# Performance work log

Hardware: AMD Instinct MI355X
Metric: run time of the kernel (lower is better)

## Reference

```python
import jax, jax.numpy as jnp
import numpy as np
import math

H, KV, D, HID, WIN = 8, 4, 256, 2048, 1024  # heads, kv heads, head_dim, hidden, sliding window
B, S = 1, 2048

def _rms(x, scale):
    # Gemma3RMSNorm: hardcoded 1e-6 eps, (1+scale) gain
    var = jnp.mean(jnp.square(x), axis=-1, keepdims=True)
    return x * jax.lax.rsqrt(var + 1e-6) * (1.0 + scale)

def _rot_half(x):
    x1, x2 = jnp.split(x, 2, axis=-1)
    return jnp.concatenate((-x2, x1), axis=-1)

def setup_inputs() -> dict:
    key = jax.random.key(0)
    ks = jax.random.split(key, 8)
    x = jax.random.normal(ks[0], (B, S, HID), jnp.float32)
    attn_mask = jnp.ones((B, S), jnp.bool_)
    segment_pos = jnp.broadcast_to(jnp.arange(S, dtype=jnp.int32)[None], (B, S))
    # true RoPE tables, theta=1e6 (Gemma3 global layers)
    inv_freq = 1.0 / (1e6 ** (np.arange(0, D, 2, dtype=np.float32) / D))
    ang = np.arange(S, dtype=np.float32)[:, None] * inv_freq[None, :]  # [S, D/2]
    emb = np.concatenate([ang, ang], axis=-1)                          # [S, D]
    cos = jnp.asarray(np.cos(emb), jnp.float32)[None]                  # [1, S, D]
    sin = jnp.asarray(np.sin(emb), jnp.float32)[None]
    sd = 1.0 / math.sqrt(HID)
    wq = jax.random.normal(ks[1], (HID, H * D), jnp.float32) * sd
    wk = jax.random.normal(ks[2], (HID, KV * D), jnp.float32) * sd
    wv = jax.random.normal(ks[3], (HID, KV * D), jnp.float32) * sd
    wo = jax.random.normal(ks[4], (H * D, HID), jnp.float32) * (1.0 / math.sqrt(H * D))
    q_scale = jnp.zeros((D,), jnp.float32)  # zeros_init as in module
    k_scale = jnp.zeros((D,), jnp.float32)
    return dict(x=x, attn_mask=attn_mask, segment_pos=segment_pos, cos=cos, sin=sin,
                wq=wq, wk=wk, wv=wv, wo=wo, q_scale=q_scale, k_scale=k_scale)

def reference(x, attn_mask, segment_pos, cos, sin, wq, wk, wv, wo, q_scale, k_scale):
    b, s, _ = x.shape
    # projections -> [b, h, s, d]
    q = (x @ wq).reshape(b, s, H, D).transpose(0, 2, 1, 3)
    k = (x @ wk).reshape(b, s, KV, D).transpose(0, 2, 1, 3)
    v = (x @ wv).reshape(b, s, KV, D).transpose(0, 2, 1, 3)
    # per-head QK RMSNorm
    q = _rms(q, q_scale)
    k = _rms(k, k_scale)
    # RoPE (cos/sin broadcast over head axis, unsqueeze_dim=1)
    c, sn = cos[:, None], sin[:, None]
    q = q * c + _rot_half(q) * sn
    k = k * c + _rot_half(k) * sn
    # GQA: repeat-interleave kv heads
    rep = H // KV
    k = jnp.repeat(k, rep, axis=1)
    v = jnp.repeat(v, rep, axis=1)
    scores = jnp.einsum('bhqd,bhkd->bhqk', q, k) / math.sqrt(D)
    # causal + padding mask (q_len > 1 path, no image bidirectional mask)
    causal = jnp.tril(jnp.ones((s, s), jnp.bool_))
    mask = causal[None] & attn_mask[:, None, :]          # [b, q, kv]
    # sliding window mask (prefill: cache positions = arange)
    kvpos = jnp.arange(s)
    pos = segment_pos[:, :, None]
    sliding = (kvpos[None, None] > pos - WIN) & (kvpos[None, None] < pos + WIN)
    full = mask & sliding
    scores = scores + jnp.where(full[:, None], 0.0, -1e37)
    w = jax.nn.softmax(scores.astype(jnp.float32), axis=-1).astype(scores.dtype)
    out = jnp.einsum('bhqk,bhkd->bhqd', w, v)
    out = out.transpose(0, 2, 1, 3).reshape(b, s, H * D)
    return out @ wo
```

## Files before the change

### kernel.cpp

```cpp
#include <hip/hip_runtime.h>
#include <hip/hip_bf16.h>

#define S_LEN 2048
#define HID 2048
#define NH 8
#define NKV 4
#define HD 256
#define WIN 1024

typedef __hip_bfloat16 bf16;
typedef __attribute__((ext_vector_type(8))) short bf16x8;
typedef __attribute__((ext_vector_type(4))) float f32x4;

__device__ __forceinline__ void gld_lds16(void* lds, const void* g) {
    __builtin_amdgcn_global_load_lds(
        (const __attribute__((address_space(1))) unsigned int*)g,
        (__attribute__((address_space(3))) unsigned int*)lds,
        16, 0, 0);
}


__device__ __forceinline__ void transT_body(const float* __restrict__ src, bf16* __restrict__ dst,
                                            int R, int C, int r0, int c0) {
    __shared__ bf16 Ts[64][72];
    const int tid = threadIdx.x;
    {
        const int r = tid >> 2;
        const int cq = (tid & 3) * 16;
#pragma unroll
        for (int j = 0; j < 16; j += 4) {
            float4 v = *(const float4*)&src[(size_t)(r0 + r) * C + c0 + cq + j];
            Ts[cq + j + 0][r] = __float2bfloat16(v.x);
            Ts[cq + j + 1][r] = __float2bfloat16(v.y);
            Ts[cq + j + 2][r] = __float2bfloat16(v.z);
            Ts[cq + j + 3][r] = __float2bfloat16(v.w);
        }
    }
    __syncthreads();
    {
        const int c = tid >> 2;
        const int rq = (tid & 3) * 16;
#pragma unroll
        for (int j = 0; j < 16; j += 8)
            *(uint4*)&dst[(size_t)(c0 + c) * R + r0 + rq + j] = *(const uint4*)&Ts[c][rq + j];
    }
}

__global__ __launch_bounds__(256)
void prep_all(const float* __restrict__ xf, const float* __restrict__ wqf,
              const float* __restrict__ wkf, const float* __restrict__ wvf,
              const float* __restrict__ wof,
              bf16* __restrict__ xb, bf16* __restrict__ wqkvt, bf16* __restrict__ wot) {
    const int bid = blockIdx.x;
    if (bid < 2048) {
        const int i = bid * 256 + threadIdx.x;
        float4 a = ((const float4*)xf)[i * 2];
        float4 b = ((const float4*)xf)[i * 2 + 1];
        union { uint4 v; bf16 h[8]; } u;
        u.h[0] = __float2bfloat16(a.x); u.h[1] = __float2bfloat16(a.y);
        u.h[2] = __float2bfloat16(a.z); u.h[3] = __float2bfloat16(a.w);
        u.h[4] = __float2bfloat16(b.x); u.h[5] = __float2bfloat16(b.y);
        u.h[6] = __float2bfloat16(b.z); u.h[7] = __float2bfloat16(b.w);
        ((uint4*)xb)[i] = u.v;
    } else if (bid < 4096) {
        const int t = bid - 2048;
        const int bx = t & 63, by = t >> 6;
        const float* src; int C, c0, drow0;
        if (bx < 32)      { src = wqf; C = 2048; c0 = bx * 64;        drow0 = bx * 64; }
        else if (bx < 48) { src = wkf; C = 1024; c0 = (bx - 32) * 64; drow0 = 2048 + (bx - 32) * 64; }
        else              { src = wvf; C = 1024; c0 = (bx - 48) * 64; drow0 = 3072 + (bx - 48) * 64; }
        bf16* dshift = wqkvt + ((size_t)drow0 - c0) * HID;
        transT_body(src, dshift, HID, C, by * 64, c0);
    } else {
        const int t = bid - 4096;
        const int bx = t & 31, by = t >> 5;
        transT_body(wof, wot, NH * HD, HID, by * 64, bx * 64);
    }
}

template<int MODE>
__global__ __launch_bounds__(512, 2)
void gemm8p(const bf16* __restrict__ A, const bf16* __restrict__ Bt,
            bf16* __restrict__ Cb,
            bf16* __restrict__ Qo, bf16* __restrict__ Ko, bf16* __restrict__ Vto) {
    extern __shared__ bf16 smem[];
    bf16* AsP = smem;
    bf16* BsP = smem + 3 * 256 * 64;

    const int tid = threadIdx.x;
    const int w = tid >> 6, lane = tid & 63;
    const int lnm = lane & 15, quad = lane >> 4;
    const int wr = w >> 1, wc = w & 1;
    const int r8 = lane >> 3;
    const int swz = ((lane & 7) ^ r8) * 8;

    const int bid = blockIdx.x;
    const int xcd = bid & 7, idx = bid >> 3;
    int m0, n0, kbeg, nt;
    size_t zoff = 0;
    if constexpr (MODE == 1) {
        const int m_t = (xcd >> 2) * 4 + (idx >> 3);
        const int n_t = (xcd & 3) * 8 + (idx & 7);
        m0 = m_t * 256; n0 = n_t * 128; kbeg = 0; nt = 2048 / 64;
    } else {
        const int z   = xcd >> 2;
        const int n_t = (xcd & 3) * 4 + (idx & 3);
        const int m_t = idx >> 2;
        m0 = m_t * 256; n0 = n_t * 128; kbeg = z * 1024; nt = 1024 / 64;
        zoff = (size_t)z * 2048 * 2048;
    }
    const int K = 2048;

    const bf16* pA[4];
#pragma unroll
    for (int g = 0; g < 4; ++g)
        pA[g] = A + (size_t)(m0 + w * 32 + g * 8 + r8) * K + kbeg + swz;
    const bf16* pB[2];
#pragma unroll
    for (int g = 0; g < 2; ++g)
        pB[g] = Bt + (size_t)(n0 + w * 16 + g * 8 + r8) * K + kbeg + swz;
    const int dA = w * 32 * 64;
    const int dB = w * 16 * 64;

#define STG_A(slot, g, t) gld_lds16(AsP + (slot) * 16384 + dA + (g) * 512, pA[g] + (t) * 64)
#define STG_B(slot, g, t) gld_lds16(BsP + (slot) * 8192  + dB + (g) * 512, pB[g] + (t) * 64)
#define LDFRAG(base, row, kh) \
    (*(const bf16x8*)((base) + (row) * 64 + (((((kh) << 2) | quad) ^ ((row) & 7)) << 3)))

    f32x4 acc[4][4];
#pragma unroll
    for (int i = 0; i < 4; ++i)
#pragma unroll
        for (int j = 0; j < 4; ++j) acc[i][j] = (f32x4){0.f, 0.f, 0.f, 0.f};

    STG_A(0, 0, 0); STG_A(0, 1, 0); STG_A(0, 2, 0); STG_A(0, 3, 0);
    STG_B(0, 0, 0); STG_B(0, 1, 0);
    STG_A(1, 0, 1); STG_A(1, 1, 1); STG_A(1, 2, 1); STG_A(1, 3, 1);
    STG_B(1, 0, 1); STG_B(1, 1, 1);
    asm volatile("s_waitcnt vmcnt(6)" ::: "memory");
    __builtin_amdgcn_sched_barrier(0);
    __builtin_amdgcn_s_barrier();

    int sc = 0;
    for (int t = 0; t < nt; ++t) {
        const int ss = (sc == 0) ? 2 : sc - 1;
        const bf16* As_ = AsP + sc * 16384;
        const bf16* Bs_ = BsP + sc * 8192;
        const bool pf = (t + 2 < nt);

        bf16x8 a0[2][2], b[4][2];
#pragma unroll
        for (int tm = 0; tm < 2; ++tm)
#pragma unroll
            for (int kh = 0; kh < 2; ++kh)
                a0[tm][kh] = LDFRAG(As_, wr * 64 + tm * 16 + lnm, kh);
#pragma unroll
        for (int tn = 0; tn < 4; ++tn)
#pragma unroll
            for (int kh = 0; kh < 2; ++kh)
                b[tn][kh] = LDFRAG(Bs_, wc * 64 + tn * 16 + lnm, kh);
        if (pf) { STG_A(ss, 0, t + 2); STG_A(ss, 1, t + 2); STG_B(ss, 0, t + 2); }
        __builtin_amdgcn_s_barrier();
        asm volatile("s_waitcnt lgkmcnt(0)" ::: "memory");
        __builtin_amdgcn_sched_barrier(0);
        __builtin_amdgcn_s_setprio(1);
#pragma unroll
        for (int kh = 0; kh < 2; ++kh)
#pragma unroll
            for (int tm = 0; tm < 2; ++tm)
#pragma unroll
                for (int tn = 0; tn < 4; ++tn)
                    acc[tm][tn] = __builtin_amdgcn_mfma_f32_16x16x32_bf16(
                        a0[tm][kh], b[tn][kh], acc[tm][tn], 0, 0, 0);
        __builtin_amdgcn_s_setprio(0);
        __builtin_amdgcn_s_barrier();

        bf16x8 a1[2][2];
#pragma unroll
        for (int tm = 0; tm < 2; ++tm)
#pragma unroll
            for (int kh = 0; kh < 2; ++kh)
                a1[tm][kh] = LDFRAG(As_, wr * 64 + (tm + 2) * 16 + lnm, kh);
        if (pf) { STG_A(ss, 2, t + 2); STG_A(ss, 3, t + 2); STG_B(ss, 1, t + 2); }
        if (pf) { asm volatile("s_waitcnt vmcnt(6)" ::: "memory"); }
        else    { asm volatile("s_waitcnt vmcnt(0)" ::: "memory"); }
        __builtin_amdgcn_sched_barrier(0);
        __builtin_amdgcn_s_barrier();
        asm volatile("s_waitcnt lgkmcnt(0)" ::: "memory");
        __builtin_amdgcn_sched_barrier(0);
        __builtin_amdgcn_s_setprio(1);
#pragma unroll
        for (int kh = 0; kh < 2; ++kh)
#pragma unroll
            for (int tm = 0; tm < 2; ++tm)
#pragma unroll
                for (int tn = 0; tn < 4; ++tn)
                    acc[tm + 2][tn] = __builtin_amdgcn_mfma_f32_16x16x32_bf16(
                        a1[tm][kh], b[tn][kh], acc[tm + 2][tn], 0, 0, 0);
        __builtin_amdgcn_s_setprio(0);
        __builtin_amdgcn_s_barrier();

        sc = (sc == 2) ? 0 : sc + 1;
    }
#undef STG_A
#undef STG_B
#undef LDFRAG

#pragma unroll
    for (int tm = 0; tm < 4; ++tm)
#pragma unroll
        for (int tn = 0; tn < 4; ++tn)
#pragma unroll
            for (int r = 0; r < 4; ++r) {
                const int row = m0 + wr * 64 + tm * 16 + quad * 4 + r;
                const int col = n0 + wc * 64 + tn * 16 + lnm;
                const float v = acc[tm][tn][r];
                if constexpr (MODE == 2) {
                    Cb[zoff + (size_t)row * 2048 + col] = __float2bfloat16(v);
                } else {
                    if (col < 2048)
                        Qo[(size_t)row * (NH * HD) + col] = __float2bfloat16(v);
                    else if (col < 3072)
                        Ko[(size_t)row * (NKV * HD) + col - 2048] = __float2bfloat16(v);
                    else
                        Vto[(size_t)(col - 3072) * S_LEN + row] = __float2bfloat16(v);
                }
            }
}

__global__ __launch_bounds__(256)
void splitk_add(const bf16* __restrict__ p, float* __restrict__ out) {
    const int i = blockIdx.x * 256 + threadIdx.x;
    union { uint4 v; bf16 h[8]; } a, b;
    a.v = ((const uint4*)p)[i];
    b.v = ((const uint4*)(p + (size_t)2048 * 2048))[i];
    float4 o0, o1;
    o0.x = (float)a.h[0] + (float)b.h[0]; o0.y = (float)a.h[1] + (float)b.h[1];
    o0.z = (float)a.h[2] + (float)b.h[2]; o0.w = (float)a.h[3] + (float)b.h[3];
    o1.x = (float)a.h[4] + (float)b.h[4]; o1.y = (float)a.h[5] + (float)b.h[5];
    o1.z = (float)a.h[6] + (float)b.h[6]; o1.w = (float)a.h[7] + (float)b.h[7];
    ((float4*)out)[i * 2]     = o0;
    ((float4*)out)[i * 2 + 1] = o1;
}

__global__ __launch_bounds__(64)
void rmsrope_kernel(bf16* __restrict__ Q, bf16* __restrict__ Kb,
                    const float* __restrict__ cosb, const float* __restrict__ sinb,
                    const float* __restrict__ qscale, const float* __restrict__ kscale,
                    float qmul) {
    const int p = blockIdx.x;
    const int hg = blockIdx.y;
    const int lane = threadIdx.x;

    bf16* base;
    const float* scale;
    float mul;
    if (hg < NH) { base = Q + (size_t)p * (NH * HD) + hg * HD; scale = qscale; mul = qmul; }
    else         { base = Kb + (size_t)p * (NKV * HD) + (hg - NH) * HD; scale = kscale; mul = 1.f; }

    const int d0 = lane * 2;
    float x0 = (float)base[d0],       x1 = (float)base[d0 + 1];
    float y0 = (float)base[d0 + 128], y1 = (float)base[d0 + 129];

    float ss = x0 * x0 + x1 * x1 + y0 * y0 + y1 * y1;
#pragma unroll
    for (int off = 32; off > 0; off >>= 1) ss += __shfl_xor(ss, off, 64);
    const float r = rsqrtf(ss * (1.0f / (float)HD) + 1e-6f);

    x0 *= r * (1.f + scale[d0]);
    x1 *= r * (1.f + scale[d0 + 1]);
    y0 *= r * (1.f + scale[d0 + 128]);
    y1 *= r * (1.f + scale[d0 + 129]);

    const size_t cb = (size_t)p * HD;
    const float c0 = cosb[cb + d0],       c1 = cosb[cb + d0 + 1];
    const float cA = cosb[cb + d0 + 128], cB = cosb[cb + d0 + 129];
    const float s0 = sinb[cb + d0],       s1 = sinb[cb + d0 + 1];
    const float sA = sinb[cb + d0 + 128], sB = sinb[cb + d0 + 129];

    base[d0]       = __float2bfloat16((x0 * c0 - y0 * s0) * mul);
    base[d0 + 1]   = __float2bfloat16((x1 * c1 - y1 * s1) * mul);
    base[d0 + 128] = __float2bfloat16((y0 * cA + x0 * sA) * mul);
    base[d0 + 129] = __float2bfloat16((y1 * cB + x1 * sB) * mul);
}

#define NCHUNK 4

__device__ __forceinline__ unsigned pkbf(float a, float b) {
    union { bf16 h; unsigned short u; } ca, cb;
    ca.h = __float2bfloat16(a); cb.h = __float2bfloat16(b);
    return (unsigned)ca.u | ((unsigned)cb.u << 16);
}

__global__ __launch_bounds__(256)
void attn_mfma(const bf16* __restrict__ Q, const bf16* __restrict__ K,
               const bf16* __restrict__ Vt, bf16* __restrict__ Op,
               float2* __restrict__ ml) {
    __shared__ bf16 Ks[2][32][256];
    __shared__ bf16 Vs[256][32];
    const int qt = blockIdx.x, h = blockIdx.y, chunk = blockIdx.z, kvh = h >> 1;
    const int tid = threadIdx.x, w = tid >> 6, lane = tid & 63;
    const int lnm = lane & 15, quad = lane >> 4;

    bf16x8 qf[8];
    const int qrow = qt * 64 + w * 16 + lnm;
#pragma unroll
    for (int s = 0; s < 8; ++s)
        qf[s] = *(const bf16x8*)&Q[(size_t)qrow * HID + h * HD + s * 32 + quad * 8];

    f32x4 o[16];
#pragma unroll
    for (int i = 0; i < 16; ++i) o[i] = (f32x4){0.f, 0.f, 0.f, 0.f};
    float M = -3e38f, L = 0.f;

    const int ktlo = (qt >= 16) ? (2 * qt - 32) : 0;
    const int kthi = 2 * qt + 1;
    const int ntile = kthi - ktlo + 1;
    const int c0 = ktlo + (chunk * ntile) / NCHUNK;
    const int c1 = ktlo + ((chunk + 1) * ntile) / NCHUNK - 1;

    const int srow = w * 8 + (lane >> 5);
    const int sunit = lane & 31;
    const bf16* kg = K + (size_t)kvh * HD;
    const int vrow = lane >> 2;
    const int vgu  = (lane & 3) ^ ((lane >> 3) & 3);
    const bf16* vsrc = Vt + ((size_t)(kvh * HD + w * 64 + vrow)) * S_LEN + vgu * 8;

#define STAGE_K(kt_, buf_)                                                        \
    {                                                                             \
        _Pragma("unroll")                                                         \
        for (int cc = 0; cc < 4; ++cc) {                                          \
            const int r_ = srow + cc * 2;                                         \
            const int ug_ = sunit ^ (r_ & 7);                                     \
            gld_lds16(&Ks[buf_][w * 8 + cc * 2][0],                               \
                      kg + (size_t)((kt_) * 32 + r_) * (NKV * HD) + ug_ * 8);     \
        }                                                                         \
    }
#define STAGE_V(kt_)                                                              \
    {                                                                             \
        _Pragma("unroll")                                                         \
        for (int cc = 0; cc < 4; ++cc)                                            \
            gld_lds16(&Vs[w * 64 + cc * 16][0],                                   \
                      vsrc + (size_t)cc * 16 * S_LEN + (kt_) * 32);               \
    }
#define KFRAG(buf_, t_, s_) \
    (*(const bf16x8*)&Ks[buf_][(t_) * 16 + lnm][((((s_) * 4 + quad) ^ (lnm & 7)) * 8)])
#define VFRAG(t2_) \
    (*(const bf16x8*)&Vs[(t2_) * 16 + lnm][(quad ^ ((lnm >> 1) & 3)) * 8])

    if (c0 <= c1) {
        STAGE_K(c0, 0);
        asm volatile("s_waitcnt vmcnt(0)" ::: "memory");
        __builtin_amdgcn_sched_barrier(0);
        __builtin_amdgcn_s_barrier();

        for (int kt = c0; kt <= c1; ++kt) {
            const int buf = (kt - c0) & 1;
            STAGE_V(kt);
            if (kt < c1) STAGE_K(kt + 1, buf ^ 1);

            f32x4 s4[2];
            s4[0] = (f32x4){0.f, 0.f, 0.f, 0.f};
            s4[1] = (f32x4){0.f, 0.f, 0.f, 0.f};
            __builtin_amdgcn_s_setprio(1);
#pragma unroll
            for (int t = 0; t < 2; ++t)
#pragma unroll
                for (int s = 0; s < 8; ++s)
                    s4[t] = __builtin_amdgcn_mfma_f32_16x16x32_bf16(
                        KFRAG(buf, t, s), qf[s], s4[t], 0, 0, 0);
            __builtin_amdgcn_s_setprio(0);

#pragma unroll
            for (int t = 0; t < 2; ++t)
#pragma unroll
                for (int r = 0; r < 4; ++r) {
                    const int n_g = kt * 32 + t * 16 + quad * 4 + r;
                    if (n_g > qrow || n_g + (WIN - 1) < qrow) s4[t][r] = -1e30f;
                }

            float mx = fmaxf(fmaxf(fmaxf(s4[0][0], s4[0][1]), fmaxf(s4[0][2], s4[0][3])),
                             fmaxf(fmaxf(s4[1][0], s4[1][1]), fmaxf(s4[1][2], s4[1][3])));
            mx = fmaxf(mx, __shfl_xor(mx, 16, 64));
            mx = fmaxf(mx, __shfl_xor(mx, 32, 64));

            if (!__all(mx <= M + 8.f)) {
                const float Mn = fmaxf(M, mx);
                const float al = __expf(M - Mn);
                M = Mn;
                L *= al;
                float alr[4];
#pragma unroll
                for (int r = 0; r < 4; ++r) alr[r] = __shfl(al, quad * 4 + r, 64);
#pragma unroll
                for (int t2 = 0; t2 < 16; ++t2)
#pragma unroll
                    for (int r = 0; r < 4; ++r) o[t2][r] *= alr[r];
            }

            float rs = 0.f;
            unsigned u00, u01, u10, u11;
            {
                float p0 = __expf(s4[0][0] - M), p1 = __expf(s4[0][1] - M);
                float p2 = __expf(s4[0][2] - M), p3 = __expf(s4[0][3] - M);
                rs += (p0 + p1) + (p2 + p3);
                u00 = pkbf(p0, p1); u01 = pkbf(p2, p3);
                p0 = __expf(s4[1][0] - M); p1 = __expf(s4[1][1] - M);
                p2 = __expf(s4[1][2] - M); p3 = __expf(s4[1][3] - M);
                rs += (p0 + p1) + (p2 + p3);
                u10 = pkbf(p0, p1); u11 = pkbf(p2, p3);
            }
            rs += __shfl_xor(rs, 16, 64);
            rs += __shfl_xor(rs, 32, 64);
            L += rs;

            const int slo = lnm + 16 * (2 * (quad & 1));
            const int shi = slo + 16;
            const int A0 = __shfl((int)u00, slo, 64), A1 = __shfl((int)u01, slo, 64);
            const int A2 = __shfl((int)u00, shi, 64), A3 = __shfl((int)u01, shi, 64);
            const int B0 = __shfl((int)u10, slo, 64), B1 = __shfl((int)u11, slo, 64);
            const int B2 = __shfl((int)u10, shi, 64), B3 = __shfl((int)u11, shi, 64);
            union { bf16x8 v; int i4[4]; } pa;
            pa.i4[0] = (quad < 2) ? A0 : B0;
            pa.i4[1] = (quad < 2) ? A1 : B1;
            pa.i4[2] = (quad < 2) ? A2 : B2;
            pa.i4[3] = (quad < 2) ? A3 : B3;

            if (kt < c1) { asm volatile("s_waitcnt vmcnt(4)" ::: "memory"); }
            else         { asm volatile("s_waitcnt vmcnt(0)" ::: "memory"); }
            __builtin_amdgcn_sched_barrier(0);
            __builtin_amdgcn_s_barrier();

            __builtin_amdgcn_s_setprio(1);
#pragma unroll
            for (int t2 = 0; t2 < 16; ++t2)
                o[t2] = __builtin_amdgcn_mfma_f32_16x16x32_bf16(pa.v, VFRAG(t2), o[t2], 0, 0, 0);
            __builtin_amdgcn_s_setprio(0);

            if (kt < c1) {
                asm volatile("s_waitcnt vmcnt(0) lgkmcnt(0)" ::: "memory");
                __builtin_amdgcn_sched_barrier(0);
                __builtin_amdgcn_s_barrier();
            }
        }
    }
#undef STAGE_K
#undef STAGE_V
#undef KFRAG
#undef VFRAG

    const float rL = (L > 0.f) ? (1.f / L) : 0.f;
    float rr[4];
#pragma unroll
    for (int r = 0; r < 4; ++r) rr[r] = __shfl(rL, quad * 4 + r, 64);
    bf16* Opc = Op + (size_t)chunk * S_LEN * HID;
#pragma unroll
    for (int t2 = 0; t2 < 16; ++t2)
#pragma unroll
        for (int r = 0; r < 4; ++r)
            Opc[(size_t)(qt * 64 + w * 16 + quad * 4 + r) * HID + h * HD + t2 * 16 + lnm] =
                __float2bfloat16(o[t2][r] * rr[r]);
    if (quad == 0)
        ml[((size_t)chunk * S_LEN + qt * 64 + w * 16 + lnm) * NH + h] = make_float2(M, L);
}

__global__ __launch_bounds__(256)
void attn_combine(const bf16* __restrict__ Op, const float2* __restrict__ ml,
                  bf16* __restrict__ O) {
    const int row = blockIdx.x, h = blockIdx.y, d = threadIdx.x;
    float2 c[NCHUNK];
    float Mx = -3e38f;
#pragma unroll
    for (int i = 0; i < NCHUNK; ++i) {
        c[i] = ml[((size_t)i * S_LEN + row) * NH + h];
        Mx = fmaxf(Mx, c[i].x);
    }
    float wsum = 0.f, wgt[NCHUNK];
#pragma unroll
    for (int i = 0; i < NCHUNK; ++i) {
        wgt[i] = c[i].y * __expf(c[i].x - Mx);
        wsum += wgt[i];
    }
    const float inv = 1.0f / wsum;
    const size_t idx = (size_t)row * HID + h * HD + d;
    float acc = 0.f;
#pragma unroll
    for (int i = 0; i < NCHUNK; ++i)
        acc += wgt[i] * (float)Op[(size_t)i * S_LEN * HID + idx];
    O[idx] = __float2bfloat16(acc * inv);
}

extern "C" void kernel_launch(void* const* d_in, const int* in_sizes, int n_in,
                              void* d_out, int out_size, void* d_ws, size_t ws_size,
                              hipStream_t stream) {
    const float* xf   = (const float*)d_in[0];
    const float* cosb = (const float*)d_in[3];
    const float* sinb = (const float*)d_in[4];
    const float* wqf  = (const float*)d_in[5];
    const float* wkf  = (const float*)d_in[6];
    const float* wvf  = (const float*)d_in[7];
    const float* wof  = (const float*)d_in[8];
    const float* qs   = (const float*)d_in[9];
    const float* ks   = (const float*)d_in[10];
    float* out = (float*)d_out;
    char* ws = (char*)d_ws;

    bf16*   wot   = (bf16*)(ws);
    bf16*   Qb    = (bf16*)(ws + ( 8ull << 20));
    bf16*   Kb    = (bf16*)(ws + (16ull << 20));
    bf16*   Vtb   = (bf16*)(ws + (20ull << 20));
    bf16*   wqkvt = (bf16*)(ws + (24ull << 20));
    bf16*   xb    = (bf16*)(ws + (40ull << 20));
    bf16*   Op    = (bf16*)(ws + (24ull << 20));
    bf16*   Ab    = (bf16*)(ws + (40ull << 20));
    bf16*   pk    = (bf16*)(ws + (24ull << 20));
    float2* ml    = (float2*)(ws + (56ull << 20));

    dim3 blk(256);

    static bool attr_done = false;
    if (!attr_done) {
        (void)hipFuncSetAttribute(reinterpret_cast<const void*>(gemm8p<1>),
                                  hipFuncAttributeMaxDynamicSharedMemorySize, 147456);
        (void)hipFuncSetAttribute(reinterpret_cast<const void*>(gemm8p<2>),
                                  hipFuncAttributeMaxDynamicSharedMemorySize, 147456);
        attr_done = true;
    }

    prep_all<<<5120, blk, 0, stream>>>(xf, wqf, wkf, wvf, wof, xb, wqkvt, wot);

    gemm8p<1><<<dim3(256), dim3(512), 147456, stream>>>(
        xb, wqkvt, nullptr, Qb, Kb, Vtb);

    rmsrope_kernel<<<dim3(S_LEN, NH + NKV), dim3(64), 0, stream>>>(
        Qb, Kb, cosb, sinb, qs, ks, 0.0625f);

    attn_mfma<<<dim3(S_LEN / 64, NH, NCHUNK), blk, 0, stream>>>(Qb, Kb, Vtb, Op, ml);
    attn_combine<<<dim3(S_LEN, NH), blk, 0, stream>>>(Op, ml, Ab);

    gemm8p<2><<<dim3(256), dim3(512), 147456, stream>>>(
        Ab, wot, pk, nullptr, nullptr, nullptr);
    splitk_add<<<2048, blk, 0, stream>>>(pk, out);
}
```

Before: 260.8 us.

## Replace QKV GEMM with split-K 256x256-tile kernel plus combine pass

The QKV projection gets a dedicated split-K (2-way) GEMM that uses 256x256 tiles, a 4-phase double-buffered LDS pipeline and 128KB of shared memory. It writes bf16 partials that a new qkv_combine kernel sums into Q, K and transposed V. The Wo weight transpose moves into its own kernel launched after the QKV GEMM, and the workspace layout is reshuffled. The goal is better tile reuse and more workgroups for the 2048x4096x2048 GEMM. In exchange it adds partial-sum traffic, an extra launch, and bf16 rounding of the partial sums.

Result: slower. 285.0 us (+9.3%).

```diff
diff --git a/kernel.cpp b/kernel.cpp
--- a/kernel.cpp
+++ b/kernel.cpp
@@ -49,8 +49,7 @@
 __global__ __launch_bounds__(256)
 void prep_all(const float* __restrict__ xf, const float* __restrict__ wqf,
               const float* __restrict__ wkf, const float* __restrict__ wvf,
-              const float* __restrict__ wof,
-              bf16* __restrict__ xb, bf16* __restrict__ wqkvt, bf16* __restrict__ wot) {
+              bf16* __restrict__ xb, bf16* __restrict__ wqkvt) {
     const int bid = blockIdx.x;
     if (bid < 2048) {
         const int i = bid * 256 + threadIdx.x;
@@ -62,7 +61,7 @@
         u.h[4] = __float2bfloat16(b.x); u.h[5] = __float2bfloat16(b.y);
         u.h[6] = __float2bfloat16(b.z); u.h[7] = __float2bfloat16(b.w);
         ((uint4*)xb)[i] = u.v;
-    } else if (bid < 4096) {
+    } else {
         const int t = bid - 2048;
         const int bx = t & 63, by = t >> 6;
         const float* src; int C, c0, drow0;
@@ -71,10 +70,201 @@
         else              { src = wvf; C = 1024; c0 = (bx - 48) * 64; drow0 = 3072 + (bx - 48) * 64; }
         bf16* dshift = wqkvt + ((size_t)drow0 - c0) * HID;
         transT_body(src, dshift, HID, C, by * 64, c0);
+    }
+}
+
+__global__ __launch_bounds__(256)
+void prep_wo(const float* __restrict__ wof, bf16* __restrict__ wot) {
+    const int bx = blockIdx.x & 31, by = blockIdx.x >> 5;
+    transT_body(wof, wot, NH * HD, HID, by * 64, bx * 64);
+}
+
+__global__ __launch_bounds__(512, 2)
+void gemm_qkv8(const bf16* __restrict__ A, const bf16* __restrict__ Bt,
+               bf16* __restrict__ P) {
+    extern __shared__ bf16 smem[];
+    const int tid = threadIdx.x;
+    const int w = tid >> 6, lane = tid & 63;
+    const int lnm = lane & 15, quad = lane >> 4;
+    const int wr = w >> 2, wc = w & 3;
+    const int K = 2048;
+    const int nt = 16;
+
+    const int bid = blockIdx.x;
+    const int xcd = bid & 7, idx = bid >> 3;
+    const int wg = xcd * 32 + idx;
+    const int z = wg >> 7;
+    const int rem = wg & 127;
+    const int m0 = (rem >> 4) * 256, n0 = (rem & 15) * 256, kbeg = z * 1024;
+
+    const int sr = lane >> 3;
+    const int su = (lane & 7) ^ sr;
+    const bf16* gA = A  + (size_t)(m0 + w * 8 + sr) * K + kbeg + su * 8;
+    const bf16* gB = Bt + (size_t)(n0 + w * 8 + sr) * K + kbeg + su * 8;
+    bf16* const lA = smem + w * 8 * 64;
+    bf16* const lB = smem + 32768 + w * 8 * 64;
+
+#define SG_A(d, c, t_) gld_lds16(lA + (d) * 16384 + (c) * 64 * 64, \
+                                 gA + (size_t)((c) * 64) * K + (t_) * 64)
+#define SG_B(d, c, t_) gld_lds16(lB + (d) * 16384 + (c) * 64 * 64, \
+                                 gB + (size_t)((c) * 64) * K + (t_) * 64)
+#define AFR(d, m, kh) (*(const bf16x8*)(smem + (d) * 16384 + \
+        (wr * 128 + (m) * 16 + lnm) * 64 + (((((kh) << 2) | quad) ^ (lnm & 7)) << 3)))
+#define BFR(d, n, kh) (*(const bf16x8*)(smem + 32768 + (d) * 16384 + \
+        (wc * 64 + (n) * 16 + lnm) * 64 + (((((kh) << 2) | quad) ^ (lnm & 7)) << 3)))
+
+    f32x4 acc[8][4];
+#pragma unroll
+    for (int i = 0; i < 8; ++i)
+#pragma unroll
+        for (int j = 0; j < 4; ++j) acc[i][j] = (f32x4){0.f, 0.f, 0.f, 0.f};
+
+    SG_A(0, 0, 0); SG_A(0, 2, 0);
+    SG_B(0, 0, 0); SG_B(0, 1, 0); SG_B(0, 2, 0); SG_B(0, 3, 0);
+    SG_A(0, 1, 0); SG_A(0, 3, 0);
+    asm volatile("s_waitcnt vmcnt(2)" ::: "memory");
+    __builtin_amdgcn_sched_barrier(0);
+    __builtin_amdgcn_s_barrier();
+
+    bf16x8 a[2][2], b[4][2];
+    for (int t = 0; t < nt; ++t) {
+        const int cur = t & 1, nxt = cur ^ 1;
+        const bool pf = (t + 1 < nt);
+
+#pragma unroll
+        for (int n = 0; n < 4; ++n)
+#pragma unroll
+            for (int kh = 0; kh < 2; ++kh) b[n][kh] = BFR(cur, n, kh);
+#pragma unroll
+        for (int m = 0; m < 2; ++m)
+#pragma unroll
+            for (int kh = 0; kh < 2; ++kh) a[m][kh] = AFR(cur, m, kh);
+        if (pf) { SG_A(nxt, 0, t + 1); SG_A(nxt, 2, t + 1); }
+        __builtin_amdgcn_s_barrier();
+        asm volatile("s_waitcnt lgkmcnt(0)" ::: "memory");
+        __builtin_amdgcn_sched_barrier(0);
+        __builtin_amdgcn_s_setprio(1);
+#pragma unroll
+        for (int kh = 0; kh < 2; ++kh)
+#pragma unroll
+            for (int m = 0; m < 2; ++m)
+#pragma unroll
+                for (int n = 0; n < 4; ++n)
+                    acc[m][n] = __builtin_amdgcn_mfma_f32_16x16x32_bf16(
+                        a[m][kh], b[n][kh], acc[m][n], 0, 0, 0);
+        __builtin_amdgcn_s_setprio(0);
+        __builtin_amdgcn_s_barrier();
+
+#pragma unroll
+        for (int m = 0; m < 2; ++m)
+#pragma unroll
+            for (int kh = 0; kh < 2; ++kh) a[m][kh] = AFR(cur, m + 2, kh);
+        if (pf) { SG_B(nxt, 0, t + 1); SG_B(nxt, 1, t + 1); }
+        __builtin_amdgcn_s_barrier();
+        asm volatile("s_waitcnt lgkmcnt(0)" ::: "memory");
+        __builtin_amdgcn_sched_barrier(0);
+        __builtin_amdgcn_s_setprio(1);
+#pragma unroll
+        for (int kh = 0; kh < 2; ++kh)
+#pragma unroll
+            for (int m = 0; m < 2; ++m)
+#pragma unroll
+                for (int n = 0; n < 4; ++n)
+                    acc[m + 2][n] = __builtin_amdgcn_mfma_f32_16x16x32_bf16(
+                        a[m][kh], b[n][kh], acc[m + 2][n], 0, 0, 0);
+        __builtin_amdgcn_s_setprio(0);
+        if (pf) { asm volatile("s_waitcnt vmcnt(4)" ::: "memory"); }
+        else    { asm volatile("s_waitcnt vmcnt(0)" ::: "memory"); }
+        __builtin_amdgcn_sched_barrier(0);
+        __builtin_amdgcn_s_barrier();
+
+#pragma unroll
+        for (int m = 0; m < 2; ++m)
+#pragma unroll
+            for (int kh = 0; kh < 2; ++kh) a[m][kh] = AFR(cur, m + 4, kh);
+        if (pf) { SG_B(nxt, 2, t + 1); SG_B(nxt, 3, t + 1); }
+        __builtin_amdgcn_s_barrier();
+        asm volatile("s_waitcnt lgkmcnt(0)" ::: "memory");
+        __builtin_amdgcn_sched_barrier(0);
+        __builtin_amdgcn_s_setprio(1);
+#pragma unroll
+        for (int kh = 0; kh < 2; ++kh)
+#pragma unroll
+            for (int m = 0; m < 2; ++m)
+#pragma unroll
+                for (int n = 0; n < 4; ++n)
+                    acc[m + 4][n] = __builtin_amdgcn_mfma_f32_16x16x32_bf16(
+                        a[m][kh], b[n][kh], acc[m + 4][n], 0, 0, 0);
+        __builtin_amdgcn_s_setprio(0);
+        __builtin_amdgcn_s_barrier();
+
+#pragma unroll
+        for (int m = 0; m < 2; ++m)
+#pragma unroll
+            for (int kh = 0; kh < 2; ++kh) a[m][kh] = AFR(cur, m + 6, kh);
+        if (pf) { SG_A(nxt, 1, t + 1); SG_A(nxt, 3, t + 1); }
+        __builtin_amdgcn_s_barrier();
+        asm volatile("s_waitcnt lgkmcnt(0)" ::: "memory");
+        __builtin_amdgcn_sched_barrier(0);
+        __builtin_amdgcn_s_setprio(1);
+#pragma unroll
+        for (int kh = 0; kh < 2; ++kh)
+#pragma unroll
+            for (int m = 0; m < 2; ++m)
+#pragma unroll
+                for (int n = 0; n < 4; ++n)
+                    acc[m + 6][n] = __builtin_amdgcn_mfma_f32_16x16x32_bf16(
+                        a[m][kh], b[n][kh], acc[m + 6][n], 0, 0, 0);
+        __builtin_amdgcn_s_setprio(0);
+        if (pf) {
+            asm volatile("s_waitcnt vmcnt(2)" ::: "memory");
+            __builtin_amdgcn_sched_barrier(0);
+        }
+        __builtin_amdgcn_s_barrier();
+    }
+#undef SG_A
+#undef SG_B
+#undef AFR
+#undef BFR
+
+    bf16* pqk = P + (size_t)z * 8388608;
+    bf16* pvt = pqk + 6291456;
+#pragma unroll
+    for (int m = 0; m < 8; ++m)
+#pragma unroll
+        for (int n = 0; n < 4; ++n)
+#pragma unroll
+            for (int r = 0; r < 4; ++r) {
+                const int row = m0 + wr * 128 + m * 16 + quad * 4 + r;
+                const int col = n0 + wc * 64 + n * 16 + lnm;
+                const float v = acc[m][n][r];
+                if (col < 3072) pqk[(size_t)row * 3072 + col] = __float2bfloat16(v);
+                else            pvt[(size_t)(col - 3072) * 2048 + row] = __float2bfloat16(v);
+            }
+}
+
+__global__ __launch_bounds__(256)
+void qkv_combine(const bf16* __restrict__ P, bf16* __restrict__ Qb,
+                 bf16* __restrict__ Kb, bf16* __restrict__ Vtb) {
+    const int bid = blockIdx.x;
+    union { uint4 v; bf16 h[8]; } a, b, o;
+    if (bid < 3072) {
+        const unsigned i = bid * 256u + threadIdx.x;
+        a.v = *(const uint4*)(P + (size_t)i * 8);
+        b.v = *(const uint4*)(P + 8388608 + (size_t)i * 8);
+        const unsigned off = i * 8u, row = off / 3072u, col = off - row * 3072u;
+        bf16* dst = (col < 2048) ? (Qb + (size_t)row * 2048 + col)
+                                 : (Kb + (size_t)row * 1024 + (col - 2048));
+#pragma unroll
+        for (int j = 0; j < 8; ++j) o.h[j] = __float2bfloat16((float)a.h[j] + (float)b.h[j]);
+        *(uint4*)dst = o.v;
     } else {
-        const int t = bid - 4096;
-        const int bx = t & 31, by = t >> 5;
-        transT_body(wof, wot, NH * HD, HID, by * 64, bx * 64);
+        const unsigned i = (bid - 3072) * 256u + threadIdx.x;
+        a.v = *(const uint4*)(P + 6291456 + (size_t)i * 8);
+        b.v = *(const uint4*)(P + 8388608 + 6291456 + (size_t)i * 8);
+#pragma unroll
+        for (int j = 0; j < 8; ++j) o.h[j] = __float2bfloat16((float)a.h[j] + (float)b.h[j]);
+        *(uint4*)(Vtb + (size_t)i * 8) = o.v;
     }
 }
 
@@ -98,11 +288,7 @@
     const int xcd = bid & 7, idx = bid >> 3;
     int m0, n0, kbeg, nt;
     size_t zoff = 0;
-    if constexpr (MODE == 1) {
-        const int m_t = (xcd >> 2) * 4 + (idx >> 3);
-        const int n_t = (xcd & 3) * 8 + (idx & 7);
-        m0 = m_t * 256; n0 = n_t * 128; kbeg = 0; nt = 2048 / 64;
-    } else {
+    {
         const int z   = xcd >> 2;
         const int n_t = (xcd & 3) * 4 + (idx & 3);
         const int m_t = idx >> 2;
@@ -214,17 +400,7 @@
             for (int r = 0; r < 4; ++r) {
                 const int row = m0 + wr * 64 + tm * 16 + quad * 4 + r;
                 const int col = n0 + wc * 64 + tn * 16 + lnm;
-                const float v = acc[tm][tn][r];
-                if constexpr (MODE == 2) {
-                    Cb[zoff + (size_t)row * 2048 + col] = __float2bfloat16(v);
-                } else {
-                    if (col < 2048)
-                        Qo[(size_t)row * (NH * HD) + col] = __float2bfloat16(v);
-                    else if (col < 3072)
-                        Ko[(size_t)row * (NKV * HD) + col - 2048] = __float2bfloat16(v);
-                    else
-                        Vto[(size_t)(col - 3072) * S_LEN + row] = __float2bfloat16(v);
-                }
+                Cb[zoff + (size_t)row * 2048 + col] = __float2bfloat16(acc[tm][tn][r]);
             }
 }
 
@@ -505,32 +681,35 @@
     float* out = (float*)d_out;
     char* ws = (char*)d_ws;
 
-    bf16*   wot   = (bf16*)(ws);
-    bf16*   Qb    = (bf16*)(ws + ( 8ull << 20));
-    bf16*   Kb    = (bf16*)(ws + (16ull << 20));
-    bf16*   Vtb   = (bf16*)(ws + (20ull << 20));
-    bf16*   wqkvt = (bf16*)(ws + (24ull << 20));
-    bf16*   xb    = (bf16*)(ws + (40ull << 20));
-    bf16*   Op    = (bf16*)(ws + (24ull << 20));
-    bf16*   Ab    = (bf16*)(ws + (40ull << 20));
-    bf16*   pk    = (bf16*)(ws + (24ull << 20));
+    bf16*   P     = (bf16*)(ws);
+    bf16*   Op    = (bf16*)(ws);
+    bf16*   pk    = (bf16*)(ws);
+    bf16*   xb    = (bf16*)(ws + (32ull << 20));
+    bf16*   Qb    = (bf16*)(ws + (32ull << 20));
+    bf16*   Ab    = (bf16*)(ws + (32ull << 20));
+    bf16*   wqkvt = (bf16*)(ws + (40ull << 20));
+    bf16*   Kb    = (bf16*)(ws + (40ull << 20));
+    bf16*   Vtb   = (bf16*)(ws + (44ull << 20));
+    bf16*   wot   = (bf16*)(ws + (48ull << 20));
     float2* ml    = (float2*)(ws + (56ull << 20));
 
     dim3 blk(256);
 
     static bool attr_done = false;
     if (!attr_done) {
-        (void)hipFuncSetAttribute(reinterpret_cast<const void*>(gemm8p<1>),
-                                  hipFuncAttributeMaxDynamicSharedMemorySize, 147456);
+        (void)hipFuncSetAttribute(reinterpret_cast<const void*>(gemm_qkv8),
+                                  hipFuncAttributeMaxDynamicSharedMemorySize, 131072);
         (void)hipFuncSetAttribute(reinterpret_cast<const void*>(gemm8p<2>),
                                   hipFuncAttributeMaxDynamicSharedMemorySize, 147456);
         attr_done = true;
     }
 
-    prep_all<<<5120, blk, 0, stream>>>(xf, wqf, wkf, wvf, wof, xb, wqkvt, wot);
-
-    gemm8p<1><<<dim3(256), dim3(512), 147456, stream>>>(
-        xb, wqkvt, nullptr, Qb, Kb, Vtb);
+    prep_all<<<4096, blk, 0, stream>>>(xf, wqf, wkf, wvf, xb, wqkvt);
+
+    gemm_qkv8<<<dim3(256), dim3(512), 131072, stream>>>(xb, wqkvt, P);
+
+    qkv_combine<<<4096, blk, 0, stream>>>(P, Qb, Kb, Vtb);
+    prep_wo<<<1024, blk, 0, stream>>>(wof, wot);
 
     rmsrope_kernel<<<dim3(S_LEN, NH + NKV), dim3(64), 0, stream>>>(
         Qb, Kb, cosb, sinb, qs, ks, 0.0625f);
```
